# Performance work log

Hardware: AMD Instinct MI355X
Metric: run time of the kernel (lower is better)

The kernel has to match this reference:

```python
import jax, jax.numpy as jnp
import numpy as np

EMBED_DIM = 768
N_HEADS = 12
HEAD_DIM = EMBED_DIM // N_HEADS
B, T = 2, 4096


def setup_inputs() -> dict:
    key = jax.random.key(0)
    k1, k2, k3, k4, k5 = jax.random.split(key, 5)
    s = 1.0 / np.sqrt(EMBED_DIM)
    return {
        "x": jax.random.normal(k1, (B, T, EMBED_DIM), dtype=jnp.float32),
        "Wqkv": jax.random.normal(k2, (EMBED_DIM, 3 * EMBED_DIM), dtype=jnp.float32) * s,
        "bqkv": jnp.zeros((3 * EMBED_DIM,), dtype=jnp.float32),
        "Wproj": jax.random.normal(k3, (EMBED_DIM, EMBED_DIM), dtype=jnp.float32) * s,
        "bproj": jnp.zeros((EMBED_DIM,), dtype=jnp.float32),
    }


def reference(x, Wqkv, bqkv, Wproj, bproj):
    Bz, Tz, C = x.shape
    qkv = x @ Wqkv + bqkv                         # [B,T,3C]
    q, k, v = jnp.split(qkv, 3, axis=2)
    # [B,T,H,D] -> [B,H,T,D]
    def heads(t):
        return t.reshape(Bz, Tz, N_HEADS, HEAD_DIM).transpose(0, 2, 1, 3)
    q, k, v = heads(q), heads(k), heads(v)
    scale = 1.0 / np.sqrt(HEAD_DIM)
    att = jnp.einsum("bhqd,bhkd->bhqk", q, k) * scale   # [B,H,T,T]
    causal = jnp.tril(jnp.ones((Tz, Tz), dtype=bool))
    att = jnp.where(causal[None, None], att, -jnp.inf)
    att = jax.nn.softmax(att, axis=-1)
    y = jnp.einsum("bhqk,bhkd->bhqd", att, v)            # [B,H,T,D]
    y = y.transpose(0, 2, 1, 3).reshape(Bz, Tz, C)
    return y @ Wproj + bproj
```

## Files before the change

### kernel.cpp

```cpp
#include <hip/hip_runtime.h>
#include <math.h>
#include <stdint.h>

typedef __attribute__((ext_vector_type(8))) short bf16x8;
typedef __attribute__((ext_vector_type(4))) float f32x4;

__device__ __forceinline__ unsigned short f2bf(float f) {
    union { float f; unsigned u; } v; v.f = f;
    return (unsigned short)((v.u + 0x7fffu + ((v.u >> 16) & 1u)) >> 16);
}

__device__ __forceinline__ void gld_lds16(const void* g, void* l) {
    __builtin_amdgcn_global_load_lds(
        (const __attribute__((address_space(1))) unsigned*)(uintptr_t)g,
        (__attribute__((address_space(3))) unsigned*)(uintptr_t)l, 16, 0, 0);
}

__global__ void k_convert(const float* __restrict__ in, unsigned short* __restrict__ out, int n4) {
    int i = blockIdx.x * blockDim.x + threadIdx.x;
    if (i >= n4) return;
    float4 f = ((const float4*)in)[i];
    ushort4 o;
    o.x = f2bf(f.x); o.y = f2bf(f.y); o.z = f2bf(f.z); o.w = f2bf(f.w);
    ((ushort4*)out)[i] = o;
}

__global__ void k_transpose(const float* __restrict__ in, unsigned short* __restrict__ out, int R, int C) {
    __shared__ float tile[32][33];
    int c0 = blockIdx.x * 32, r0 = blockIdx.y * 32;
    int tx = threadIdx.x, ty = threadIdx.y;
#pragma unroll
    for (int i = 0; i < 4; ++i)
        tile[ty + i * 8][tx] = in[(size_t)(r0 + ty + i * 8) * C + c0 + tx];
    __syncthreads();
#pragma unroll
    for (int i = 0; i < 4; ++i)
        out[(size_t)(c0 + ty + i * 8) * R + r0 + tx] = f2bf(tile[tx][ty + i * 8]);
}

#define LDT 32

__device__ __forceinline__ void gemm_core(
    const unsigned short* __restrict__ A, const unsigned short* __restrict__ Bt,
    int K, unsigned short* As, unsigned short* Bs, f32x4 (&acc)[4][4])
{
    const int tid  = threadIdx.x;
    const int lane = tid & 63;
    const int w    = tid >> 6;
    const int wm   = (w >> 1) * 64, wn = (w & 1) * 64;
    const int l15  = lane & 15, quad = lane >> 4;
    const int m0 = blockIdx.x * 128, n0 = blockIdx.y * 128;

    const f32x4 zero = {0.f, 0.f, 0.f, 0.f};
#pragma unroll
    for (int i = 0; i < 4; ++i)
#pragma unroll
        for (int j = 0; j < 4; ++j) acc[i][j] = zero;

    const int r0 = tid >> 2, p8 = (tid & 3) * 8;
    const unsigned short* Ag0 = A  + (size_t)(m0 + r0) * K + p8;
    const unsigned short* Ag1 = A  + (size_t)(m0 + r0 + 64) * K + p8;
    const unsigned short* Bg0 = Bt + (size_t)(n0 + r0) * K + p8;
    const unsigned short* Bg1 = Bt + (size_t)(n0 + r0 + 64) * K + p8;
    unsigned short* lA0 = As + r0 * LDT + p8;
    unsigned short* lA1 = lA0 + 64 * LDT;
    unsigned short* lB0 = Bs + r0 * LDT + p8;
    unsigned short* lB1 = lB0 + 64 * LDT;

    const int nk = K >> 5;
    for (int kt = 0; kt < nk; ++kt) {
        __syncthreads();
        gld_lds16(Ag0, lA0);
        gld_lds16(Ag1, lA1);
        gld_lds16(Bg0, lB0);
        gld_lds16(Bg1, lB1);
        Ag0 += 32; Ag1 += 32; Bg0 += 32; Bg1 += 32;
        __syncthreads();
        bf16x8 af[4], bfr[4];
#pragma unroll
        for (int mi = 0; mi < 4; ++mi)
            af[mi] = *(const bf16x8*)&As[(wm + mi * 16 + l15) * LDT + quad * 8];
#pragma unroll
        for (int nj = 0; nj < 4; ++nj)
            bfr[nj] = *(const bf16x8*)&Bs[(wn + nj * 16 + l15) * LDT + quad * 8];
#pragma unroll
        for (int mi = 0; mi < 4; ++mi)
#pragma unroll
            for (int nj = 0; nj < 4; ++nj)
                acc[mi][nj] = __builtin_amdgcn_mfma_f32_16x16x32_bf16(af[mi], bfr[nj], acc[mi][nj], 0, 0, 0);
    }
}

__global__ __launch_bounds__(256) void k_gemm_qkv(
    const unsigned short* __restrict__ A, const unsigned short* __restrict__ Bt,
    const float* __restrict__ bias,
    unsigned short* __restrict__ QL, unsigned short* __restrict__ KL,
    unsigned short* __restrict__ VL)
{
    __shared__ __align__(16) unsigned short As[128 * LDT];
    __shared__ __align__(16) unsigned short Bs[128 * LDT];
    f32x4 acc[4][4];
    gemm_core(A, Bt, 768, As, Bs, acc);

    const int tid = threadIdx.x, lane = tid & 63, w = tid >> 6;
    const int wm = (w >> 1) * 64, wn = (w & 1) * 64;
    const int l15 = lane & 15, quad = lane >> 4;
    const int m0 = blockIdx.x * 128, n0 = blockIdx.y * 128;
    const float cscale = 0.18033688011f;
#pragma unroll
    for (int nj = 0; nj < 4; ++nj) {
        int cg = n0 + wn + nj * 16 + l15;
        float bv = bias[cg];
        int which = cg / 768;
        int rem = cg - which * 768;
        int hd = rem >> 6, d = rem & 63;
        float sc = (which == 0) ? cscale : 1.0f;
#pragma unroll
        for (int mi = 0; mi < 4; ++mi) {
#pragma unroll
            for (int r = 0; r < 4; ++r) {
                int rg = m0 + wm + mi * 16 + quad * 4 + r;
                int b = rg >> 12, tk = rg & 4095;
                int bh = b * 12 + hd;
                unsigned short ob = f2bf((acc[mi][nj][r] + bv) * sc);
                if (which == 0) {
                    size_t idx = ((((size_t)bh * 128 + (tk >> 5)) * 2 + ((tk >> 4) & 1)) * 2 + (d >> 5)) * 512
                               + ((d >> 3) & 3) * 128 + (tk & 15) * 8 + (d & 7);
                    QL[idx] = ob;
                } else if (which == 1) {
                    size_t idx = ((((size_t)bh * 64 + (tk >> 6)) * 4 + ((tk >> 4) & 3)) * 2 + (d >> 5)) * 512
                               + ((d >> 3) & 3) * 128 + (tk & 15) * 8 + (d & 7);
                    KL[idx] = ob;
                } else {
                    int wi = tk & 63;
                    size_t idx = ((((size_t)bh * 64 + (tk >> 6)) * 4 + (d >> 4)) * 2 + (wi >> 5)) * 512
                               + ((wi >> 3) & 3) * 128 + (d & 15) * 8 + (wi & 7);
                    VL[idx] = ob;
                }
            }
        }
    }
}

__global__ __launch_bounds__(256) void k_gemm_proj(
    const unsigned short* __restrict__ A, const unsigned short* __restrict__ Bt,
    const float* __restrict__ bias, float* __restrict__ out)
{
    __shared__ __align__(16) unsigned short As[128 * LDT];
    __shared__ __align__(16) unsigned short Bs[128 * LDT];
    f32x4 acc[4][4];
    gemm_core(A, Bt, 768, As, Bs, acc);

    const int tid = threadIdx.x, lane = tid & 63, w = tid >> 6;
    const int wm = (w >> 1) * 64, wn = (w & 1) * 64;
    const int l15 = lane & 15, quad = lane >> 4;
    const int m0 = blockIdx.x * 128, n0 = blockIdx.y * 128;
#pragma unroll
    for (int nj = 0; nj < 4; ++nj) {
        int cg = n0 + wn + nj * 16 + l15;
        float bv = bias[cg];
#pragma unroll
        for (int mi = 0; mi < 4; ++mi)
#pragma unroll
            for (int r = 0; r < 4; ++r) {
                int rg = m0 + wm + mi * 16 + quad * 4 + r;
                out[(size_t)rg * 768 + cg] = acc[mi][nj][r] + bv;
            }
    }
}

#define LDP 72

__global__ __launch_bounds__(256) void k_attn(
    const unsigned short* __restrict__ QL, const unsigned short* __restrict__ KL,
    const unsigned short* __restrict__ VL, unsigned short* __restrict__ Y)
{
    __shared__ __align__(16) char smem[30720];
    unsigned short* Ps = (unsigned short*)smem;
    float* Cb = (float*)smem;

    const int tid = threadIdx.x, lane = tid & 63;
    const int w = __builtin_amdgcn_readfirstlane(tid >> 6);
    const int l15 = lane & 15, quad = lane >> 4;
    const int id = blockIdx.x;
    const int bh = id % 24;
    const int qi = 127 - id / 24;
    const int q0 = qi * 32;
    const int nkt = qi / 2 + 1;
    const int lo = (nkt * w) >> 2, hi = (nkt * (w + 1)) >> 2;
    unsigned short* Pw = Ps + w * 32 * LDP;

    unsigned short* pwb = Pw + l15 * LDP + quad * 4;
    const unsigned short* prb = Pw + l15 * LDP + quad * 8;

    const unsigned short* Qb = QL + (((size_t)bh * 128 + qi) * 4) * 512 + lane * 8;
    const unsigned short* kp = KL + ((size_t)bh * 64 + lo) * 8 * 512 + lane * 8;
    const unsigned short* vp = VL + ((size_t)bh * 64 + lo) * 8 * 512 + lane * 8;

    bf16x8 qt[2][2];
#pragma unroll
    for (int m = 0; m < 2; ++m)
#pragma unroll
        for (int h = 0; h < 2; ++h)
            qt[m][h] = *(const bf16x8*)(Qb + (m * 2 + h) * 512);

    const f32x4 zero = {0.f, 0.f, 0.f, 0.f};
    f32x4 O[2][4], lac[2];
#pragma unroll
    for (int m = 0; m < 2; ++m) {
        lac[m] = zero;
#pragma unroll
        for (int dj = 0; dj < 4; ++dj) O[m][dj] = zero;
    }

    const short ONE = (short)0x3F80;
    const bf16x8 onesf = {ONE, ONE, ONE, ONE, ONE, ONE, ONE, ONE};

    if (lo < hi) {
        bf16x8 ka[4][2];
#pragma unroll
        for (int i = 0; i < 4; ++i)
#pragma unroll
            for (int h = 0; h < 2; ++h)
                ka[i][h] = *(const bf16x8*)(kp + (i * 2 + h) * 512);

        for (int kt = lo; kt < hi; ++kt) {
            f32x4 st[2][4];
#pragma unroll
            for (int i = 0; i < 4; ++i)
#pragma unroll
                for (int m = 0; m < 2; ++m) {
                    f32x4 z = __builtin_amdgcn_mfma_f32_16x16x32_bf16(ka[i][0], qt[m][0], zero, 0, 0, 0);
                    st[m][i] = __builtin_amdgcn_mfma_f32_16x16x32_bf16(ka[i][1], qt[m][1], z, 0, 0, 0);
                }

            bf16x8 vf[4][2];
#pragma unroll
            for (int dj = 0; dj < 4; ++dj)
#pragma unroll
                for (int h = 0; h < 2; ++h)
                    vf[dj][h] = *(const bf16x8*)(vp + (dj * 2 + h) * 512);
            vp += 8 * 512;

            if (kt + 1 < hi) {
                kp += 8 * 512;
#pragma unroll
                for (int i = 0; i < 4; ++i)
#pragma unroll
                    for (int h = 0; h < 2; ++h)
                        ka[i][h] = *(const bf16x8*)(kp + (i * 2 + h) * 512);
            }

            if (kt == nkt - 1) {
                const int kb = kt * 64;
#pragma unroll
                for (int m = 0; m < 2; ++m)
#pragma unroll
                    for (int i = 0; i < 4; ++i)
#pragma unroll
                        for (int r = 0; r < 4; ++r)
                            if (kb + i * 16 + quad * 4 + r > q0 + m * 16 + l15)
                                st[m][i][r] = -INFINITY;
            }

#pragma unroll
            for (int m = 0; m < 2; ++m)
#pragma unroll
                for (int i = 0; i < 4; ++i) {
                    unsigned e0 = __float_as_uint(__builtin_amdgcn_exp2f(fminf(st[m][i][0], 80.f))) + 0x8000u;
                    unsigned e1 = __float_as_uint(__builtin_amdgcn_exp2f(fminf(st[m][i][1], 80.f))) + 0x8000u;
                    unsigned e2 = __float_as_uint(__builtin_amdgcn_exp2f(fminf(st[m][i][2], 80.f))) + 0x8000u;
                    unsigned e3 = __float_as_uint(__builtin_amdgcn_exp2f(fminf(st[m][i][3], 80.f))) + 0x8000u;
                    uint2 pk;
                    pk.x = __builtin_amdgcn_perm(e1, e0, 0x07060302);
                    pk.y = __builtin_amdgcn_perm(e3, e2, 0x07060302);
                    *(uint2*)(pwb + m * 16 * LDP + i * 16) = pk;
                }

            bf16x8 pa[2][2];
#pragma unroll
            for (int m = 0; m < 2; ++m) {
                pa[m][0] = *(const bf16x8*)(prb + m * 16 * LDP);
                pa[m][1] = *(const bf16x8*)(prb + m * 16 * LDP + 32);
            }

#pragma unroll
            for (int m = 0; m < 2; ++m) {
                f32x4 z = __builtin_amdgcn_mfma_f32_16x16x32_bf16(pa[m][0], onesf, lac[m], 0, 0, 0);
                lac[m] = __builtin_amdgcn_mfma_f32_16x16x32_bf16(pa[m][1], onesf, z, 0, 0, 0);
            }
#pragma unroll
            for (int dj = 0; dj < 4; ++dj)
#pragma unroll
                for (int m = 0; m < 2; ++m) {
                    f32x4 z = __builtin_amdgcn_mfma_f32_16x16x32_bf16(pa[m][0], vf[dj][0], O[m][dj], 0, 0, 0);
                    O[m][dj] = __builtin_amdgcn_mfma_f32_16x16x32_bf16(pa[m][1], vf[dj][1], z, 0, 0, 0);
                }
        }
    }

    __syncthreads();
    if (w > 0) {
        float* Ow = Cb + (w - 1) * 2560;
#pragma unroll
        for (int m = 0; m < 2; ++m) {
#pragma unroll
            for (int dj = 0; dj < 4; ++dj)
                *(f32x4*)&Ow[(m * 4 + dj) * 256 + lane * 4] = O[m][dj];
            *(f32x4*)&Ow[2048 + m * 256 + lane * 4] = lac[m];
        }
    }
    __syncthreads();
    if (w == 0) {
#pragma unroll
        for (int c = 0; c < 3; ++c) {
            const float* Ow = Cb + c * 2560;
#pragma unroll
            for (int m = 0; m < 2; ++m) {
#pragma unroll
                for (int dj = 0; dj < 4; ++dj)
                    O[m][dj] += *(const f32x4*)&Ow[(m * 4 + dj) * 256 + lane * 4];
                lac[m] += *(const f32x4*)&Ow[2048 + m * 256 + lane * 4];
            }
        }
        const int b = bh / 12, hd = bh % 12;
#pragma unroll
        for (int m = 0; m < 2; ++m)
#pragma unroll
            for (int r = 0; r < 4; ++r) {
                float inv = 1.0f / lac[m][r];
                int t = q0 + 16 * m + quad * 4 + r;
                size_t base = ((size_t)(b * 4096 + t)) * 768 + hd * 64;
#pragma unroll
                for (int dj = 0; dj < 4; ++dj)
                    Y[base + dj * 16 + l15] = f2bf(O[m][dj][r] * inv);
            }
    }
}

extern "C" void kernel_launch(void* const* d_in, const int* in_sizes, int n_in,
                              void* d_out, int out_size, void* d_ws, size_t ws_size,
                              hipStream_t stream) {
    (void)in_sizes; (void)n_in; (void)out_size; (void)ws_size;
    const float* x     = (const float*)d_in[0];
    const float* Wqkv  = (const float*)d_in[1];
    const float* bqkv  = (const float*)d_in[2];
    const float* Wproj = (const float*)d_in[3];
    const float* bproj = (const float*)d_in[4];
    float* out = (float*)d_out;

    char* ws = (char*)d_ws;
    size_t off = 0;
    auto alloc = [&](size_t bytes) -> void* {
        void* p = ws + off;
        off += (bytes + 255) & ~(size_t)255;
        return p;
    };
    unsigned short* xb     = (unsigned short*)alloc((size_t)8192 * 768 * 2);
    unsigned short* WqkvT  = (unsigned short*)alloc((size_t)2304 * 768 * 2);
    unsigned short* WprojT = (unsigned short*)alloc((size_t)768 * 768 * 2);
    unsigned short* QLb    = (unsigned short*)alloc((size_t)24 * 4096 * 64 * 2);
    unsigned short* KLb    = (unsigned short*)alloc((size_t)24 * 4096 * 64 * 2);
    unsigned short* VLb    = (unsigned short*)alloc((size_t)24 * 4096 * 64 * 2);
    unsigned short* Yb     = (unsigned short*)alloc((size_t)8192 * 768 * 2);

    k_convert<<<6144, 256, 0, stream>>>(x, xb, 8192 * 768 / 4);
    dim3 tb(32, 8);
    k_transpose<<<dim3(72, 24), tb, 0, stream>>>(Wqkv, WqkvT, 768, 2304);
    k_transpose<<<dim3(24, 24), tb, 0, stream>>>(Wproj, WprojT, 768, 768);
    k_gemm_qkv<<<dim3(64, 18), 256, 0, stream>>>(xb, WqkvT, bqkv, QLb, KLb, VLb);
    k_attn<<<dim3(3072), 256, 0, stream>>>(QLb, KLb, VLb, Yb);
    k_gemm_proj<<<dim3(64, 6), 256, 0, stream>>>(Yb, WprojT, bproj, out);
}
```

Baseline: 262.2 us.

## Software-pipeline attention loop with double-buffered P tiles and prefetched K/V

Restructures the attention inner loop so QK^T and exp for the next key tile are computed after issuing the PV MFMAs for the current tile, with a double-buffered per-wave P buffer in LDS. K and V loads are prefetched one iteration ahead, the LDS row pitch changes from 72 to 68, and the fminf clamp before exp2 is dropped. This is meant to overlap MFMA, exp, LDS and global-load latency, but it raises register and LDS pressure. Without the clamp, large scores could overflow exp2.

```diff
diff --git a/kernel.cpp b/kernel.cpp
--- a/kernel.cpp
+++ b/kernel.cpp
@@ -169,13 +169,13 @@
     }
 }
 
-#define LDP 72
+#define LDP 68
 
 __global__ __launch_bounds__(256) void k_attn(
     const unsigned short* __restrict__ QL, const unsigned short* __restrict__ KL,
     const unsigned short* __restrict__ VL, unsigned short* __restrict__ Y)
 {
-    __shared__ __align__(16) char smem[30720];
+    __shared__ __align__(16) char smem[34816];
     unsigned short* Ps = (unsigned short*)smem;
     float* Cb = (float*)smem;
 
@@ -188,14 +188,14 @@
     const int q0 = qi * 32;
     const int nkt = qi / 2 + 1;
     const int lo = (nkt * w) >> 2, hi = (nkt * (w + 1)) >> 2;
-    unsigned short* Pw = Ps + w * 32 * LDP;
-
-    unsigned short* pwb = Pw + l15 * LDP + quad * 4;
-    const unsigned short* prb = Pw + l15 * LDP + quad * 8;
+    unsigned short* Pw = Ps + w * 2 * 32 * LDP;
+
+    const int pw_off = l15 * LDP + quad * 4;
+    const int pr_off = l15 * LDP + quad * 8;
 
     const unsigned short* Qb = QL + (((size_t)bh * 128 + qi) * 4) * 512 + lane * 8;
-    const unsigned short* kp = KL + ((size_t)bh * 64 + lo) * 8 * 512 + lane * 8;
-    const unsigned short* vp = VL + ((size_t)bh * 64 + lo) * 8 * 512 + lane * 8;
+    const unsigned short* kp = KL + ((size_t)bh * 64 + lo) * 4096 + lane * 8;
+    const unsigned short* vp = VL + ((size_t)bh * 64 + lo) * 4096 + lane * 8;
 
     bf16x8 qt[2][2];
 #pragma unroll
@@ -217,14 +217,19 @@
     const bf16x8 onesf = {ONE, ONE, ONE, ONE, ONE, ONE, ONE, ONE};
 
     if (lo < hi) {
-        bf16x8 ka[4][2];
+        bf16x8 ka[4][2], vf[4][2];
 #pragma unroll
         for (int i = 0; i < 4; ++i)
 #pragma unroll
             for (int h = 0; h < 2; ++h)
                 ka[i][h] = *(const bf16x8*)(kp + (i * 2 + h) * 512);
-
-        for (int kt = lo; kt < hi; ++kt) {
+#pragma unroll
+        for (int dj = 0; dj < 4; ++dj)
+#pragma unroll
+            for (int h = 0; h < 2; ++h)
+                vf[dj][h] = *(const bf16x8*)(vp + (dj * 2 + h) * 512);
+
+        {
             f32x4 st[2][4];
 #pragma unroll
             for (int i = 0; i < 4; ++i)
@@ -233,26 +238,8 @@
                     f32x4 z = __builtin_amdgcn_mfma_f32_16x16x32_bf16(ka[i][0], qt[m][0], zero, 0, 0, 0);
                     st[m][i] = __builtin_amdgcn_mfma_f32_16x16x32_bf16(ka[i][1], qt[m][1], z, 0, 0, 0);
                 }
-
-            bf16x8 vf[4][2];
-#pragma unroll
-            for (int dj = 0; dj < 4; ++dj)
-#pragma unroll
-                for (int h = 0; h < 2; ++h)
-                    vf[dj][h] = *(const bf16x8*)(vp + (dj * 2 + h) * 512);
-            vp += 8 * 512;
-
-            if (kt + 1 < hi) {
-                kp += 8 * 512;
-#pragma unroll
-                for (int i = 0; i < 4; ++i)
-#pragma unroll
-                    for (int h = 0; h < 2; ++h)
-                        ka[i][h] = *(const bf16x8*)(kp + (i * 2 + h) * 512);
-            }
-
-            if (kt == nkt - 1) {
-                const int kb = kt * 64;
+            if (lo == nkt - 1) {
+                const int kb = lo * 64;
 #pragma unroll
                 for (int m = 0; m < 2; ++m)
 #pragma unroll
@@ -262,26 +249,40 @@
                             if (kb + i * 16 + quad * 4 + r > q0 + m * 16 + l15)
                                 st[m][i][r] = -INFINITY;
             }
-
 #pragma unroll
             for (int m = 0; m < 2; ++m)
 #pragma unroll
                 for (int i = 0; i < 4; ++i) {
-                    unsigned e0 = __float_as_uint(__builtin_amdgcn_exp2f(fminf(st[m][i][0], 80.f))) + 0x8000u;
-                    unsigned e1 = __float_as_uint(__builtin_amdgcn_exp2f(fminf(st[m][i][1], 80.f))) + 0x8000u;
-                    unsigned e2 = __float_as_uint(__builtin_amdgcn_exp2f(fminf(st[m][i][2], 80.f))) + 0x8000u;
-                    unsigned e3 = __float_as_uint(__builtin_amdgcn_exp2f(fminf(st[m][i][3], 80.f))) + 0x8000u;
+                    unsigned e0 = __float_as_uint(__builtin_amdgcn_exp2f(st[m][i][0])) + 0x8000u;
+                    unsigned e1 = __float_as_uint(__builtin_amdgcn_exp2f(st[m][i][1])) + 0x8000u;
+                    unsigned e2 = __float_as_uint(__builtin_amdgcn_exp2f(st[m][i][2])) + 0x8000u;
+                    unsigned e3 = __float_as_uint(__builtin_amdgcn_exp2f(st[m][i][3])) + 0x8000u;
                     uint2 pk;
                     pk.x = __builtin_amdgcn_perm(e1, e0, 0x07060302);
                     pk.y = __builtin_amdgcn_perm(e3, e2, 0x07060302);
-                    *(uint2*)(pwb + m * 16 * LDP + i * 16) = pk;
+                    *(uint2*)(Pw + pw_off + m * 16 * LDP + i * 16) = pk;
                 }
+        }
+
+        for (int kt = lo; kt < hi; ++kt) {
+            unsigned short* bc = Pw + ((kt - lo) & 1) * 32 * LDP;
+            unsigned short* bn = Pw + (((kt - lo) & 1) ^ 1) * 32 * LDP;
+            const bool more = (kt + 1 < hi);
 
             bf16x8 pa[2][2];
 #pragma unroll
             for (int m = 0; m < 2; ++m) {
-                pa[m][0] = *(const bf16x8*)(prb + m * 16 * LDP);
-                pa[m][1] = *(const bf16x8*)(prb + m * 16 * LDP + 32);
+                pa[m][0] = *(const bf16x8*)(bc + pr_off + m * 16 * LDP);
+                pa[m][1] = *(const bf16x8*)(bc + pr_off + m * 16 * LDP + 32);
+            }
+
+            if (more) {
+                kp += 4096;
+#pragma unroll
+                for (int i = 0; i < 4; ++i)
+#pragma unroll
+                    for (int h = 0; h < 2; ++h)
+                        ka[i][h] = *(const bf16x8*)(kp + (i * 2 + h) * 512);
             }
 
 #pragma unroll
@@ -296,6 +297,48 @@
                     f32x4 z = __builtin_amdgcn_mfma_f32_16x16x32_bf16(pa[m][0], vf[dj][0], O[m][dj], 0, 0, 0);
                     O[m][dj] = __builtin_amdgcn_mfma_f32_16x16x32_bf16(pa[m][1], vf[dj][1], z, 0, 0, 0);
                 }
+
+            if (more) {
+                vp += 4096;
+#pragma unroll
+                for (int dj = 0; dj < 4; ++dj)
+#pragma unroll
+                    for (int h = 0; h < 2; ++h)
+                        vf[dj][h] = *(const bf16x8*)(vp + (dj * 2 + h) * 512);
+
+                f32x4 st[2][4];
+#pragma unroll
+                for (int i = 0; i < 4; ++i)
+#pragma unroll
+                    for (int m = 0; m < 2; ++m) {
+                        f32x4 z = __builtin_amdgcn_mfma_f32_16x16x32_bf16(ka[i][0], qt[m][0], zero, 0, 0, 0);
+                        st[m][i] = __builtin_amdgcn_mfma_f32_16x16x32_bf16(ka[i][1], qt[m][1], z, 0, 0, 0);
+                    }
+                if (kt + 1 == nkt - 1) {
+                    const int kb = (kt + 1) * 64;
+#pragma unroll
+                    for (int m = 0; m < 2; ++m)
+#pragma unroll
+                        for (int i = 0; i < 4; ++i)
+#pragma unroll
+                            for (int r = 0; r < 4; ++r)
+                                if (kb + i * 16 + quad * 4 + r > q0 + m * 16 + l15)
+                                    st[m][i][r] = -INFINITY;
+                }
+#pragma unroll
+                for (int m = 0; m < 2; ++m)
+#pragma unroll
+                    for (int i = 0; i < 4; ++i) {
+                        unsigned e0 = __float_as_uint(__builtin_amdgcn_exp2f(st[m][i][0])) + 0x8000u;
+                        unsigned e1 = __float_as_uint(__builtin_amdgcn_exp2f(st[m][i][1])) + 0x8000u;
+                        unsigned e2 = __float_as_uint(__builtin_amdgcn_exp2f(st[m][i][2])) + 0x8000u;
+                        unsigned e3 = __float_as_uint(__builtin_amdgcn_exp2f(st[m][i][3])) + 0x8000u;
+                        uint2 pk;
+                        pk.x = __builtin_amdgcn_perm(e1, e0, 0x07060302);
+                        pk.y = __builtin_amdgcn_perm(e3, e2, 0x07060302);
+                        *(uint2*)(bn + pw_off + m * 16 * LDP + i * 16) = pk;
+                    }
+            }
         }
     }
 
```

Result: faster. 255.3 us (-2.6%).
